# Kernel tuning notes

Hardware: AMD Instinct MI355X
Metric: run time of the kernel (lower is better)

Reference implementation:

```python
import jax, jax.numpy as jnp
import numpy as np

B, S, D = 2, 2048, 2048
H = 16
NOPE, ROPE, DV = 128, 64, 128
DQK = NOPE + ROPE  # 192
QLR, KVLR = 1536, 512


def setup_inputs() -> dict:
    key = jax.random.key(0)
    ks = jax.random.split(key, 8)
    hidden_states = jax.random.normal(ks[0], (B, S, D), dtype=jnp.float32) * 0.02
    sequence_mask = jnp.ones((B, S), dtype=bool)
    # rotary frequencies (complex exponential split into cos/sin), theta=10000
    inv_freq = 1.0 / (10000.0 ** (np.arange(0, ROPE, 2, dtype=np.float32) / ROPE))
    angles = np.outer(np.arange(S, dtype=np.float32), inv_freq)  # [S, ROPE//2]
    freqs_cos = jnp.asarray(np.cos(angles), dtype=jnp.float32)
    freqs_sin = jnp.asarray(np.sin(angles), dtype=jnp.float32)
    def lin(k, fan_in, fan_out):
        return jax.random.normal(k, (fan_in, fan_out), dtype=jnp.float32) / np.sqrt(fan_in)
    return {
        'hidden_states': hidden_states,
        'sequence_mask': sequence_mask,
        'freqs_cos': freqs_cos,
        'freqs_sin': freqs_sin,
        'Wq_down': lin(ks[1], D, QLR),
        'Wkv_down': lin(ks[2], D, KVLR + ROPE),
        'Wq_up': lin(ks[3], QLR, H * DQK),
        'Wkv_up': lin(ks[4], KVLR, H * (DV + NOPE)),
        'Wo': lin(ks[5], H * DV, D),
    }


def _rmsnorm(x, eps=1e-5):
    return x * jax.lax.rsqrt(jnp.mean(x * x, axis=-1, keepdims=True) + eps)


def _apply_rope(x, cos, sin):
    # x: [B,S,H,d] with interleaved (real, imag) pairs; cos/sin: [S, d//2]
    b, s, h, d = x.shape
    xr = x.reshape(b, s, h, d // 2, 2)
    x0, x1 = xr[..., 0], xr[..., 1]
    c = cos[None, :s, None, :]
    sn = sin[None, :s, None, :]
    y = jnp.stack([x0 * c - x1 * sn, x0 * sn + x1 * c], axis=-1)
    return y.reshape(b, s, h, d)


def reference(hidden_states, sequence_mask, freqs_cos, freqs_sin,
              Wq_down, Wkv_down, Wq_up, Wkv_up, Wo):
    b, s, _ = hidden_states.shape
    # Q path: down-project -> rmsnorm -> up-project
    q_latent = _rmsnorm(hidden_states @ Wq_down)
    q = (q_latent @ Wq_up).reshape(b, s, H, DQK)
    q_nope, q_rope = q[..., :NOPE], q[..., NOPE:]
    q_rope = _apply_rope(q_rope, freqs_cos, freqs_sin)
    q = jnp.concatenate([q_rope, q_nope], axis=-1)  # [B,S,H,DQK]
    # KV path
    kvdr = hidden_states @ Wkv_down  # [B,S,KVLR+ROPE]
    kv_latent, k_rope = kvdr[..., :KVLR], kvdr[..., KVLR:]
    k_rope = _apply_rope(k_rope.reshape(b, s, 1, ROPE), freqs_cos, freqs_sin)
    k_rope = jnp.broadcast_to(k_rope, (b, s, H, ROPE))
    kv = _rmsnorm(kv_latent) @ Wkv_up  # [B,S,H*(NOPE+DV)]
    k_nope = kv[..., :H * NOPE].reshape(b, s, H, NOPE)
    v = kv[..., H * NOPE:].reshape(b, s, H, DV)
    k = jnp.concatenate([k_rope, k_nope], axis=-1)  # [B,S,H,DQK]
    # causal attention (flash_attn_varlen with full masks == per-batch causal)
    scale = 1.0 / np.sqrt(DQK)
    scores = jnp.einsum('bqhd,bkhd->bhqk', q, k) * scale
    causal = jnp.tril(jnp.ones((s, s), dtype=bool))
    mask = causal[None, None, :, :] & sequence_mask[:, None, None, :]
    scores = jnp.where(mask, scores, jnp.float32(-1e9))
    attn = jax.nn.softmax(scores, axis=-1)
    out = jnp.einsum('bhqk,bkhd->bqhd', attn, v).reshape(b, s, H * DV)
    return out @ Wo
```

## Files before the change

kernel.cpp:

```cpp
#include <hip/hip_runtime.h>
#include <math.h>


typedef unsigned short u16;
typedef __attribute__((ext_vector_type(8))) __bf16 bf16x8;
typedef __attribute__((ext_vector_type(4))) float f32x4;

#define DEV static __device__ __forceinline__

DEV float b2f(u16 v) { return __uint_as_float(((unsigned int)v) << 16); }
DEV u16 f2b(float f) {
  unsigned int u = __float_as_uint(f);
  u += 0x7fffu + ((u >> 16) & 1u);
  return (u16)(u >> 16);
}

DEV float waveReduceSum(float v) {
  #pragma unroll
  for (int o = 32; o > 0; o >>= 1) v += __shfl_down(v, o, 64);
  return v;
}

DEV void gld16(const u16* g, u16* l) {
  __builtin_amdgcn_global_load_lds((const __attribute__((address_space(1))) void*)g,
                                   (__attribute__((address_space(3))) void*)l, 16, 0, 0);
}

__global__ __launch_bounds__(256)
void cvt_f32_bf16(const float* __restrict__ in, u16* __restrict__ out, int n4) {
  int i = blockIdx.x * 256 + threadIdx.x;
  if (i < n4) {
    float4 v = reinterpret_cast<const float4*>(in)[i];
    ushort4 o;
    o.x = f2b(v.x); o.y = f2b(v.y); o.z = f2b(v.z); o.w = f2b(v.w);
    reinterpret_cast<ushort4*>(out)[i] = o;
  }
}

__global__ __launch_bounds__(256)
void transpose_f32_bf16(const float* __restrict__ in, u16* __restrict__ out, int R, int C) {
  __shared__ u16 tile[32][33];
  int c0 = blockIdx.x * 32, r0 = blockIdx.y * 32;
  for (int i = threadIdx.y; i < 32; i += 8)
    tile[i][threadIdx.x] = f2b(in[(size_t)(r0 + i) * C + c0 + threadIdx.x]);
  __syncthreads();
  for (int i = threadIdx.y; i < 32; i += 8)
    out[(size_t)(c0 + i) * R + r0 + threadIdx.x] = tile[threadIdx.x][i];
}

template<int OUT_BF16>
__global__ __launch_bounds__(256)
void gemm_bt(const u16* __restrict__ A, const u16* __restrict__ BT, void* __restrict__ Cp,
             int M, int N, int K) {
  __shared__ __attribute__((aligned(16))) u16 As[4096];
  __shared__ __attribute__((aligned(16))) u16 Bs[4096];
  const int tid = threadIdx.x;
  const int lane = tid & 63;
  const int wave = tid >> 6;
  const int wm = (wave >> 1) * 64;
  const int wn = (wave & 1) * 64;
  const int q = lane >> 4;
  const int l16 = lane & 15;

  const int gx = gridDim.x;
  const int nwg = gx * gridDim.y;
  const int orig = blockIdx.y * gx + blockIdx.x;
  const int cpx = nwg >> 3;
  const int swz = (orig & 7) * cpx + (orig >> 3);
  const int bm = (swz / gx) * 128;
  const int bn = (swz % gx) * 128;

  f32x4 zero = {0.f, 0.f, 0.f, 0.f};
  f32x4 acc[4][4];
  #pragma unroll
  for (int i = 0; i < 4; i++)
    #pragma unroll
    for (int j = 0; j < 4; j++) acc[i][j] = zero;

  for (int k0 = 0; k0 < K; k0 += 32) {
    #pragma unroll
    for (int i = 0; i < 2; i++) {
      int jb = i * 256 + wave * 64;
      int u = jb + lane;
      int row = u >> 2;
      int kq = (u & 3) ^ ((u >> 3) & 3);
      gld16(A + (size_t)(bm + row) * K + k0 + kq * 8, As + jb * 8);
      int rB = bn + row;
      if (rB >= N) rB = N - 1;
      gld16(BT + (size_t)rB * K + k0 + kq * 8, Bs + jb * 8);
    }
    __syncthreads();
    bf16x8 af[4], bfr[4];
    #pragma unroll
    for (int t = 0; t < 4; t++) {
      int rowA = wm + t * 16 + l16;
      int rowB = wn + t * 16 + l16;
      int uA = (rowA << 2) | (q ^ ((rowA >> 1) & 3));
      int uB = (rowB << 2) | (q ^ ((rowB >> 1) & 3));
      af[t]  = *reinterpret_cast<const bf16x8*>(As + uA * 8);
      bfr[t] = *reinterpret_cast<const bf16x8*>(Bs + uB * 8);
    }
    #pragma unroll
    for (int mt = 0; mt < 4; mt++)
      #pragma unroll
      for (int nt = 0; nt < 4; nt++)
        acc[mt][nt] = __builtin_amdgcn_mfma_f32_16x16x32_bf16(af[mt], bfr[nt], acc[mt][nt], 0, 0, 0);
    __syncthreads();
  }

  float* Cf = (float*)Cp;
  u16* Cb = (u16*)Cp;
  #pragma unroll
  for (int mt = 0; mt < 4; mt++) {
    #pragma unroll
    for (int nt = 0; nt < 4; nt++) {
      int col = bn + wn + nt * 16 + l16;
      if (col < N) {
        int row0 = bm + wm + mt * 16 + q * 4;
        #pragma unroll
        for (int r = 0; r < 4; r++) {
          size_t idx = (size_t)(row0 + r) * N + col;
          float v = acc[mt][nt][r];
          if (OUT_BF16) Cb[idx] = f2b(v); else Cf[idx] = v;
        }
      }
    }
  }
}

__global__ __launch_bounds__(256)
void rmsnorm_rows(const float* __restrict__ in, u16* __restrict__ out, int C, int stride) {
  int row = blockIdx.x;
  const float* x = in + (size_t)row * stride;
  float ss = 0.f;
  for (int i = threadIdx.x; i < C; i += 256) { float v = x[i]; ss += v * v; }
  ss = waveReduceSum(ss);
  __shared__ float red[4];
  __shared__ float s_scale;
  int lane = threadIdx.x & 63, wid = threadIdx.x >> 6;
  if (lane == 0) red[wid] = ss;
  __syncthreads();
  if (threadIdx.x == 0)
    s_scale = rsqrtf((red[0] + red[1] + red[2] + red[3]) / (float)C + 1e-5f);
  __syncthreads();
  float sc = s_scale;
  u16* o = out + (size_t)row * C;
  for (int i = threadIdx.x; i < C; i += 256) o[i] = f2b(x[i] * sc);
}

__global__ __launch_bounds__(256)
void rope_pack_q(const u16* __restrict__ q2, const float* __restrict__ fc, const float* __restrict__ fs,
                 u16* __restrict__ Q) {
  const float scale = 0.07216878364870323f;
  int bs = blockIdx.x;
  int b = bs >> 11, s = bs & 2047;
  __shared__ float c[32], sn[32];
  if (threadIdx.x < 32) {
    c[threadIdx.x] = fc[s * 32 + threadIdx.x];
    sn[threadIdx.x] = fs[s * 32 + threadIdx.x];
  }
  __syncthreads();
  const u16* qrow = q2 + (size_t)bs * 3072;
  for (int t = threadIdx.x; t < 512; t += 256) {
    int h = t >> 5, i = t & 31;
    float x0 = b2f(qrow[h * 192 + 128 + 2 * i]);
    float x1 = b2f(qrow[h * 192 + 128 + 2 * i + 1]);
    size_t base = ((size_t)(b * 16 + h) * 2048 + s) * 192;
    Q[base + 2 * i]     = f2b((x0 * c[i] - x1 * sn[i]) * scale);
    Q[base + 2 * i + 1] = f2b((x0 * sn[i] + x1 * c[i]) * scale);
  }
  for (int t = threadIdx.x; t < 2048; t += 256) {
    int h = t >> 7, j = t & 127;
    Q[((size_t)(b * 16 + h) * 2048 + s) * 192 + 64 + j] = f2b(b2f(qrow[h * 192 + j]) * scale);
  }
}

__global__ __launch_bounds__(256)
void kv_split(const float* __restrict__ t13, const float* __restrict__ fc, const float* __restrict__ fs,
              u16* __restrict__ kvl, u16* __restrict__ krope) {
  int row = blockIdx.x;
  int s = row & 2047;
  const float* x = t13 + (size_t)row * 2112 + 1536;
  float ss = 0.f;
  for (int i = threadIdx.x; i < 512; i += 256) { float v = x[i]; ss += v * v; }
  ss = waveReduceSum(ss);
  __shared__ float red[4];
  __shared__ float s_scale;
  int lane = threadIdx.x & 63, wid = threadIdx.x >> 6;
  if (lane == 0) red[wid] = ss;
  __syncthreads();
  if (threadIdx.x == 0)
    s_scale = rsqrtf((red[0] + red[1] + red[2] + red[3]) * (1.0f / 512.0f) + 1e-5f);
  __syncthreads();
  float sc = s_scale;
  for (int i = threadIdx.x; i < 512; i += 256) kvl[(size_t)row * 512 + i] = f2b(x[i] * sc);
  if (threadIdx.x < 32) {
    int i = threadIdx.x;
    float cc = fc[s * 32 + i], sn = fs[s * 32 + i];
    float x0 = x[512 + 2 * i], x1 = x[512 + 2 * i + 1];
    krope[(size_t)row * 64 + 2 * i]     = f2b(x0 * cc - x1 * sn);
    krope[(size_t)row * 64 + 2 * i + 1] = f2b(x0 * sn + x1 * cc);
  }
}

__global__ __launch_bounds__(256)
void assemble_kv2(const u16* __restrict__ kvb, const u16* __restrict__ krope,
                  u16* __restrict__ Kc, u16* __restrict__ Vt) {
  int ks = blockIdx.x;
  int bh = blockIdx.y;
  int b = bh >> 4, h = bh & 15;
  int t = threadIdx.x;
  if (t < 192) {
    int kq = t >> 3, sl = t & 7;
    int s = ks * 8 + sl;
    size_t bs = (size_t)(b * 2048 + s);
    uint4 v;
    if (kq < 8) v = *reinterpret_cast<const uint4*>(krope + bs * 64 + kq * 8);
    else        v = *reinterpret_cast<const uint4*>(kvb + bs * 4096 + h * 128 + (kq - 8) * 8);
    *reinterpret_cast<uint4*>(Kc + (((size_t)bh * 24 + kq) * 2048 + s) * 8) = v;
  }
  if (t < 128) {
    int dv = t;
    u16 tmp[8];
    #pragma unroll
    for (int j = 0; j < 8; j++) {
      int s = ks * 8 + j;
      tmp[j] = kvb[(size_t)(b * 2048 + s) * 4096 + 2048 + h * 128 + dv];
    }
    *reinterpret_cast<uint4*>(Vt + (((size_t)bh * 256 + ks) * 128 + dv) * 8) = *reinterpret_cast<uint4*>(tmp);
  }
}

__global__ __launch_bounds__(256, 2)
void flash_attn7(const u16* __restrict__ Q, const u16* __restrict__ Kc,
                 const u16* __restrict__ Vt, u16* __restrict__ O) {
  __shared__ __attribute__((aligned(16))) u16 Ks[2][24 * 64 * 8];
  __shared__ __attribute__((aligned(16))) u16 Vs[8 * 128 * 8];
  __shared__ __attribute__((aligned(16))) u16 Ps[4 * 16 * 72];

  const int blk = blockIdx.x;
  const int bh = ((blk & 7) << 2) | (blk >> 7);
  const int tpair = (blk >> 3) & 15;
  const int b = bh >> 4, h = bh & 15;
  const int tid = threadIdx.x, lane = tid & 63, wave = tid >> 6;
  const int quad = lane >> 4, l16 = lane & 15;
  u16* PsW = Ps + wave * 16 * 72;

  bf16x8 onesf;
  #pragma unroll
  for (int j = 0; j < 8; j++) onesf[j] = (l16 == 0) ? (__bf16)1.0f : (__bf16)0.0f;

  auto stageK = [&](u16* KsB, int kk) {
    #pragma unroll
    for (int ii = 0; ii < 6; ii++) {
      int kq = wave * 6 + ii;
      gld16(Kc + (((size_t)bh * 24 + kq) * 2048 + kk + lane) * 8, KsB + kq * 64 * 8);
    }
  };
  auto stageV = [&](int kk) {
    #pragma unroll
    for (int jj = 0; jj < 4; jj++) {
      int vc = wave * 4 + jj, kc = vc >> 1, dvh = vc & 1;
      gld16(Vt + (((size_t)bh * 256 + (kk >> 3) + kc) * 128 + dvh * 64 + lane) * 8,
            Vs + (kc * 128 + dvh * 64) * 8);
    }
  };

  for (int phase = 0; phase < 2; phase++) {
    const int qt = phase == 0 ? tpair : 31 - tpair;
    const int q0 = qt * 64;
    const int nk = (qt + 1) * 64;

    bf16x8 qf[6];
    {
      int qrow = q0 + wave * 16 + l16;
      const u16* qp = Q + ((size_t)bh * 2048 + qrow) * 192 + quad * 8;
      #pragma unroll
      for (int kc = 0; kc < 6; kc++)
        qf[kc] = *reinterpret_cast<const bf16x8*>(qp + kc * 32);
    }

    f32x4 zero = {0.f, 0.f, 0.f, 0.f};
    f32x4 oacc[9];
    #pragma unroll
    for (int nt = 0; nt < 9; nt++) oacc[nt] = zero;

    for (int k0 = 0; k0 < nk; k0 += 64) {
      const int cur = (k0 >> 6) & 1;
      const bool hasnext = (k0 + 64 < nk);

      __builtin_amdgcn_s_barrier();
      __builtin_amdgcn_sched_barrier(0);
      if (k0 == 0) stageK(Ks[0], 0);
      stageV(k0);
      if (hasnext) {
        stageK(Ks[cur ^ 1], k0 + 64);
        asm volatile("s_waitcnt vmcnt(10)" ::: "memory");
      } else {
        asm volatile("s_waitcnt vmcnt(4)" ::: "memory");
      }
      __builtin_amdgcn_sched_barrier(0);
      __builtin_amdgcn_s_barrier();
      __builtin_amdgcn_sched_barrier(0);

      const u16* KsC = Ks[cur];

      f32x4 sacc[4];
      #pragma unroll
      for (int nt = 0; nt < 4; nt++) sacc[nt] = zero;
      #pragma unroll
      for (int kc = 0; kc < 6; kc++) {
        #pragma unroll
        for (int nt = 0; nt < 4; nt++) {
          bf16x8 kb = *reinterpret_cast<const bf16x8*>(KsC + ((kc * 4 + quad) * 64 + nt * 16 + l16) * 8);
          sacc[nt] = __builtin_amdgcn_mfma_f32_16x16x32_bf16(qf[kc], kb, sacc[nt], 0, 0, 0);
        }
      }

      #pragma unroll
      for (int r = 0; r < 4; r++) {
        int qrow_g = q0 + wave * 16 + quad * 4 + r;
        #pragma unroll
        for (int nt = 0; nt < 4; nt++) {
          int key = k0 + nt * 16 + l16;
          float p = (key <= qrow_g) ? __expf(sacc[nt][r]) : 0.f;
          PsW[(quad * 4 + r) * 72 + nt * 16 + l16] = f2b(p);
        }
      }

      if (hasnext) asm volatile("s_waitcnt vmcnt(6)" ::: "memory");
      else         asm volatile("s_waitcnt vmcnt(0)" ::: "memory");
      __builtin_amdgcn_sched_barrier(0);
      __builtin_amdgcn_s_barrier();
      __builtin_amdgcn_sched_barrier(0);

      #pragma unroll
      for (int kcp = 0; kcp < 2; kcp++) {
        bf16x8 pa = *reinterpret_cast<const bf16x8*>(PsW + l16 * 72 + kcp * 32 + quad * 8);
        #pragma unroll
        for (int nt = 0; nt < 8; nt++) {
          bf16x8 vb = *reinterpret_cast<const bf16x8*>(Vs + ((kcp * 4 + quad) * 128 + nt * 16 + l16) * 8);
          oacc[nt] = __builtin_amdgcn_mfma_f32_16x16x32_bf16(pa, vb, oacc[nt], 0, 0, 0);
        }
        oacc[8] = __builtin_amdgcn_mfma_f32_16x16x32_bf16(pa, onesf, oacc[8], 0, 0, 0);
      }
    }

    #pragma unroll
    for (int r = 0; r < 4; r++) {
      float l = __shfl(oacc[8][r], lane & 48, 64);
      float inv = 1.0f / l;
      int s = q0 + wave * 16 + quad * 4 + r;
      #pragma unroll
      for (int nt = 0; nt < 8; nt++)
        O[((size_t)b * 2048 + s) * 2048 + h * 128 + nt * 16 + l16] = f2b(oacc[nt][r] * inv);
    }
  }
}

extern "C" void kernel_launch(void* const* d_in, const int* in_sizes, int n_in,
                              void* d_out, int out_size, void* d_ws, size_t ws_size,
                              hipStream_t stream) {
  (void)in_sizes; (void)n_in; (void)out_size; (void)ws_size;
  const float* hs   = (const float*)d_in[0];
  const float* fc   = (const float*)d_in[2];
  const float* fs   = (const float*)d_in[3];
  const float* Wqd  = (const float*)d_in[4];
  const float* Wkvd = (const float*)d_in[5];
  const float* Wqu  = (const float*)d_in[6];
  const float* Wkvu = (const float*)d_in[7];
  const float* Wo   = (const float*)d_in[8];

  char* ws = (char*)d_ws;
  size_t off = 0;
  auto alloc = [&](size_t bytes) { size_t o = off; off += (bytes + 255) & ~(size_t)255; return o; };
  const size_t oHS   = alloc(16777216);
  const size_t oRA   = alloc(16777216);
  const size_t oRB   = alloc(25165824);
  const size_t oRC   = alloc(12582912);
  const size_t oRD   = alloc(25165824);
  const size_t oRE   = alloc(34603008);
  const size_t oKVL  = alloc(4194304);
  const size_t oKR   = alloc(524288);
  const size_t oW13T  = alloc(8650752);
  const size_t oWquT  = alloc(9437184);
  const size_t oWkvuT = alloc(4194304);
  const size_t oWoT   = alloc(8388608);

  u16* hs_bf = (u16*)(ws + oHS);
  u16* Vt   = (u16*)(ws + oRA);
  u16* q2   = (u16*)(ws + oRB);
  u16* Kc   = (u16*)(ws + oRB);
  u16* qlat = (u16*)(ws + oRC);
  u16* Qb   = (u16*)(ws + oRD);
  float* t13 = (float*)(ws + oRE);
  u16* kvb  = (u16*)(ws + oRE);
  u16* attn_out = (u16*)(ws + oRE);
  u16* kvl  = (u16*)(ws + oKVL);
  u16* krope = (u16*)(ws + oKR);
  u16* W13T  = (u16*)(ws + oW13T);
  u16* WquT  = (u16*)(ws + oWquT);
  u16* WkvuT = (u16*)(ws + oWkvuT);
  u16* WoT   = (u16*)(ws + oWoT);

  cvt_f32_bf16<<<8192, 256, 0, stream>>>(hs, hs_bf, 2097152);
  dim3 tb(32, 8);
  transpose_f32_bf16<<<dim3(48, 64), tb, 0, stream>>>(Wqd, W13T, 2048, 1536);
  transpose_f32_bf16<<<dim3(18, 64), tb, 0, stream>>>(Wkvd, W13T + (size_t)1536 * 2048, 2048, 576);
  transpose_f32_bf16<<<dim3(96, 48), tb, 0, stream>>>(Wqu, WquT, 1536, 3072);
  transpose_f32_bf16<<<dim3(128, 16), tb, 0, stream>>>(Wkvu, WkvuT, 512, 4096);
  transpose_f32_bf16<<<dim3(64, 64), tb, 0, stream>>>(Wo, WoT, 2048, 2048);

  gemm_bt<0><<<dim3(17, 32), 256, 0, stream>>>(hs_bf, W13T, t13, 4096, 2112, 2048);
  rmsnorm_rows<<<4096, 256, 0, stream>>>(t13, qlat, 1536, 2112);
  gemm_bt<1><<<dim3(24, 32), 256, 0, stream>>>(qlat, WquT, q2, 4096, 3072, 1536);
  rope_pack_q<<<4096, 256, 0, stream>>>(q2, fc, fs, Qb);
  kv_split<<<4096, 256, 0, stream>>>(t13, fc, fs, kvl, krope);
  gemm_bt<1><<<dim3(32, 32), 256, 0, stream>>>(kvl, WkvuT, kvb, 4096, 4096, 512);
  assemble_kv2<<<dim3(256, 32), 256, 0, stream>>>(kvb, krope, Kc, Vt);
  flash_attn7<<<dim3(512), 256, 0, stream>>>(Qb, Kc, Vt, attn_out);
  gemm_bt<0><<<dim3(16, 32), 256, 0, stream>>>(attn_out, WoT, (float*)d_out, 4096, 2048, 2048);
}
```

Before: 470.7 us.

## Merge launches, fuse norm kernels, and use exp2 with a mask fast path in attention

Result: faster. 446.2 us (-5.2%).

```diff
diff --git a/kernel.cpp b/kernel.cpp
--- a/kernel.cpp
+++ b/kernel.cpp
@@ -7,12 +7,24 @@
 typedef __attribute__((ext_vector_type(4))) float f32x4;
 
 #define DEV static __device__ __forceinline__
+
+#if __has_builtin(__builtin_amdgcn_exp2f)
+#define EXP2(x) __builtin_amdgcn_exp2f(x)
+#else
+#define EXP2(x) exp2f(x)
+#endif
 
 DEV float b2f(u16 v) { return __uint_as_float(((unsigned int)v) << 16); }
 DEV u16 f2b(float f) {
   unsigned int u = __float_as_uint(f);
   u += 0x7fffu + ((u >> 16) & 1u);
   return (u16)(u >> 16);
+}
+DEV u16 f2b_hw(float f) {
+  __bf16 h = (__bf16)f;
+  u16 r;
+  __builtin_memcpy(&r, &h, 2);
+  return r;
 }
 
 DEV float waveReduceSum(float v) {
@@ -38,9 +50,20 @@
 }
 
 __global__ __launch_bounds__(256)
-void transpose_f32_bf16(const float* __restrict__ in, u16* __restrict__ out, int R, int C) {
+void transpose_all(const float* __restrict__ Wqd, const float* __restrict__ Wkvd,
+                   const float* __restrict__ Wqu, const float* __restrict__ Wkvu,
+                   const float* __restrict__ Wo,
+                   u16* __restrict__ W13T, u16* __restrict__ WquT,
+                   u16* __restrict__ WkvuT, u16* __restrict__ WoT) {
   __shared__ u16 tile[32][33];
-  int c0 = blockIdx.x * 32, r0 = blockIdx.y * 32;
+  int n = blockIdx.x;
+  const float* in; u16* out; int R, C, gx, local;
+  if (n < 3072)       { in = Wqd;  out = W13T;                        R = 2048; C = 1536; gx = 48;  local = n; }
+  else if (n < 4224)  { in = Wkvd; out = W13T + (size_t)1536 * 2048;  R = 2048; C = 576;  gx = 18;  local = n - 3072; }
+  else if (n < 8832)  { in = Wqu;  out = WquT;                        R = 1536; C = 3072; gx = 96;  local = n - 4224; }
+  else if (n < 10880) { in = Wkvu; out = WkvuT;                       R = 512;  C = 4096; gx = 128; local = n - 8832; }
+  else                { in = Wo;   out = WoT;                         R = 2048; C = 2048; gx = 64;  local = n - 10880; }
+  int c0 = (local % gx) * 32, r0 = (local / gx) * 32;
   for (int i = threadIdx.y; i < 32; i += 8)
     tile[i][threadIdx.x] = f2b(in[(size_t)(r0 + i) * C + c0 + threadIdx.x]);
   __syncthreads();
@@ -49,11 +72,8 @@
 }
 
 template<int OUT_BF16>
-__global__ __launch_bounds__(256)
-void gemm_bt(const u16* __restrict__ A, const u16* __restrict__ BT, void* __restrict__ Cp,
-             int M, int N, int K) {
-  __shared__ __attribute__((aligned(16))) u16 As[4096];
-  __shared__ __attribute__((aligned(16))) u16 Bs[4096];
+DEV void gemm_body(const u16* __restrict__ A, const u16* __restrict__ BT, void* __restrict__ Cp,
+                   int N, int K, int gx, int nwg, int orig, u16* As, u16* Bs) {
   const int tid = threadIdx.x;
   const int lane = tid & 63;
   const int wave = tid >> 6;
@@ -62,9 +82,6 @@
   const int q = lane >> 4;
   const int l16 = lane & 15;
 
-  const int gx = gridDim.x;
-  const int nwg = gx * gridDim.y;
-  const int orig = blockIdx.y * gx + blockIdx.x;
   const int cpx = nwg >> 3;
   const int swz = (orig & 7) * cpx + (orig >> 3);
   const int bm = (swz / gx) * 128;
@@ -128,30 +145,76 @@
   }
 }
 
-__global__ __launch_bounds__(256)
-void rmsnorm_rows(const float* __restrict__ in, u16* __restrict__ out, int C, int stride) {
-  int row = blockIdx.x;
-  const float* x = in + (size_t)row * stride;
-  float ss = 0.f;
-  for (int i = threadIdx.x; i < C; i += 256) { float v = x[i]; ss += v * v; }
-  ss = waveReduceSum(ss);
+template<int OUT_BF16>
+__global__ __launch_bounds__(256)
+void gemm_bt(const u16* __restrict__ A, const u16* __restrict__ BT, void* __restrict__ Cp,
+             int N, int K) {
+  __shared__ __attribute__((aligned(16))) u16 As[4096];
+  __shared__ __attribute__((aligned(16))) u16 Bs[4096];
+  const int gx = gridDim.x;
+  const int nwg = gx * gridDim.y;
+  const int orig = blockIdx.y * gx + blockIdx.x;
+  gemm_body<OUT_BF16>(A, BT, Cp, N, K, gx, nwg, orig, As, Bs);
+}
+
+__global__ __launch_bounds__(256)
+void gemm_up2(const u16* __restrict__ qlat, const u16* __restrict__ WquT, u16* __restrict__ q2,
+              const u16* __restrict__ kvl, const u16* __restrict__ WkvuT, u16* __restrict__ kvb) {
+  __shared__ __attribute__((aligned(16))) u16 As[4096];
+  __shared__ __attribute__((aligned(16))) u16 Bs[4096];
+  int n = blockIdx.x;
+  if (n < 768) gemm_body<1>(qlat, WquT, q2, 3072, 1536, 24, 768, n, As, Bs);
+  else         gemm_body<1>(kvl, WkvuT, kvb, 4096, 512, 32, 1024, n - 768, As, Bs);
+}
+
+__global__ __launch_bounds__(256)
+void norm_split(const float* __restrict__ t13, const float* __restrict__ fc, const float* __restrict__ fs,
+                u16* __restrict__ qlat, u16* __restrict__ kvl, u16* __restrict__ krope) {
   __shared__ float red[4];
   __shared__ float s_scale;
   int lane = threadIdx.x & 63, wid = threadIdx.x >> 6;
-  if (lane == 0) red[wid] = ss;
-  __syncthreads();
-  if (threadIdx.x == 0)
-    s_scale = rsqrtf((red[0] + red[1] + red[2] + red[3]) / (float)C + 1e-5f);
-  __syncthreads();
-  float sc = s_scale;
-  u16* o = out + (size_t)row * C;
-  for (int i = threadIdx.x; i < C; i += 256) o[i] = f2b(x[i] * sc);
+  if (blockIdx.x < 4096) {
+    int row = blockIdx.x;
+    const float* x = t13 + (size_t)row * 2112;
+    float ss = 0.f;
+    for (int i = threadIdx.x; i < 1536; i += 256) { float v = x[i]; ss += v * v; }
+    ss = waveReduceSum(ss);
+    if (lane == 0) red[wid] = ss;
+    __syncthreads();
+    if (threadIdx.x == 0)
+      s_scale = rsqrtf((red[0] + red[1] + red[2] + red[3]) * (1.0f / 1536.0f) + 1e-5f);
+    __syncthreads();
+    float sc = s_scale;
+    u16* o = qlat + (size_t)row * 1536;
+    for (int i = threadIdx.x; i < 1536; i += 256) o[i] = f2b(x[i] * sc);
+  } else {
+    int row = blockIdx.x - 4096;
+    int s = row & 2047;
+    const float* x = t13 + (size_t)row * 2112 + 1536;
+    float ss = 0.f;
+    for (int i = threadIdx.x; i < 512; i += 256) { float v = x[i]; ss += v * v; }
+    ss = waveReduceSum(ss);
+    if (lane == 0) red[wid] = ss;
+    __syncthreads();
+    if (threadIdx.x == 0)
+      s_scale = rsqrtf((red[0] + red[1] + red[2] + red[3]) * (1.0f / 512.0f) + 1e-5f);
+    __syncthreads();
+    float sc = s_scale;
+    for (int i = threadIdx.x; i < 512; i += 256) kvl[(size_t)row * 512 + i] = f2b(x[i] * sc);
+    if (threadIdx.x < 32) {
+      int i = threadIdx.x;
+      float cc = fc[s * 32 + i], sn = fs[s * 32 + i];
+      float x0 = x[512 + 2 * i], x1 = x[512 + 2 * i + 1];
+      krope[(size_t)row * 64 + 2 * i]     = f2b(x0 * cc - x1 * sn);
+      krope[(size_t)row * 64 + 2 * i + 1] = f2b(x0 * sn + x1 * cc);
+    }
+  }
 }
 
 __global__ __launch_bounds__(256)
 void rope_pack_q(const u16* __restrict__ q2, const float* __restrict__ fc, const float* __restrict__ fs,
                  u16* __restrict__ Q) {
-  const float scale = 0.07216878364870323f;
+  const float scale = 0.10411756711f;
   int bs = blockIdx.x;
   int b = bs >> 11, s = bs & 2047;
   __shared__ float c[32], sn[32];
@@ -172,34 +235,6 @@
   for (int t = threadIdx.x; t < 2048; t += 256) {
     int h = t >> 7, j = t & 127;
     Q[((size_t)(b * 16 + h) * 2048 + s) * 192 + 64 + j] = f2b(b2f(qrow[h * 192 + j]) * scale);
-  }
-}
-
-__global__ __launch_bounds__(256)
-void kv_split(const float* __restrict__ t13, const float* __restrict__ fc, const float* __restrict__ fs,
-              u16* __restrict__ kvl, u16* __restrict__ krope) {
-  int row = blockIdx.x;
-  int s = row & 2047;
-  const float* x = t13 + (size_t)row * 2112 + 1536;
-  float ss = 0.f;
-  for (int i = threadIdx.x; i < 512; i += 256) { float v = x[i]; ss += v * v; }
-  ss = waveReduceSum(ss);
-  __shared__ float red[4];
-  __shared__ float s_scale;
-  int lane = threadIdx.x & 63, wid = threadIdx.x >> 6;
-  if (lane == 0) red[wid] = ss;
-  __syncthreads();
-  if (threadIdx.x == 0)
-    s_scale = rsqrtf((red[0] + red[1] + red[2] + red[3]) * (1.0f / 512.0f) + 1e-5f);
-  __syncthreads();
-  float sc = s_scale;
-  for (int i = threadIdx.x; i < 512; i += 256) kvl[(size_t)row * 512 + i] = f2b(x[i] * sc);
-  if (threadIdx.x < 32) {
-    int i = threadIdx.x;
-    float cc = fc[s * 32 + i], sn = fs[s * 32 + i];
-    float x0 = x[512 + 2 * i], x1 = x[512 + 2 * i + 1];
-    krope[(size_t)row * 64 + 2 * i]     = f2b(x0 * cc - x1 * sn);
-    krope[(size_t)row * 64 + 2 * i + 1] = f2b(x0 * sn + x1 * cc);
   }
 }
 
@@ -232,7 +267,7 @@
 }
 
 __global__ __launch_bounds__(256, 2)
-void flash_attn7(const u16* __restrict__ Q, const u16* __restrict__ Kc,
+void flash_attn8(const u16* __restrict__ Q, const u16* __restrict__ Kc,
                  const u16* __restrict__ Vt, u16* __restrict__ O) {
   __shared__ __attribute__((aligned(16))) u16 Ks[2][24 * 64 * 8];
   __shared__ __attribute__((aligned(16))) u16 Vs[8 * 128 * 8];
@@ -317,14 +352,26 @@
         }
       }
 
-      #pragma unroll
-      for (int r = 0; r < 4; r++) {
-        int qrow_g = q0 + wave * 16 + quad * 4 + r;
+      if (k0 + 63 <= q0 + wave * 16) {
         #pragma unroll
-        for (int nt = 0; nt < 4; nt++) {
-          int key = k0 + nt * 16 + l16;
-          float p = (key <= qrow_g) ? __expf(sacc[nt][r]) : 0.f;
-          PsW[(quad * 4 + r) * 72 + nt * 16 + l16] = f2b(p);
+        for (int r = 0; r < 4; r++) {
+          #pragma unroll
+          for (int nt = 0; nt < 4; nt++) {
+            float p = EXP2(sacc[nt][r]);
+            PsW[(quad * 4 + r) * 72 + nt * 16 + l16] = f2b_hw(p);
+          }
+        }
+      } else {
+        #pragma unroll
+        for (int r = 0; r < 4; r++) {
+          int qrow_g = q0 + wave * 16 + quad * 4 + r;
+          #pragma unroll
+          for (int nt = 0; nt < 4; nt++) {
+            int key = k0 + nt * 16 + l16;
+            float e = EXP2(sacc[nt][r]);
+            float p = (key <= qrow_g) ? e : 0.f;
+            PsW[(quad * 4 + r) * 72 + nt * 16 + l16] = f2b_hw(p);
+          }
         }
       }
 
@@ -404,20 +451,13 @@
   u16* WoT   = (u16*)(ws + oWoT);
 
   cvt_f32_bf16<<<8192, 256, 0, stream>>>(hs, hs_bf, 2097152);
-  dim3 tb(32, 8);
-  transpose_f32_bf16<<<dim3(48, 64), tb, 0, stream>>>(Wqd, W13T, 2048, 1536);
-  transpose_f32_bf16<<<dim3(18, 64), tb, 0, stream>>>(Wkvd, W13T + (size_t)1536 * 2048, 2048, 576);
-  transpose_f32_bf16<<<dim3(96, 48), tb, 0, stream>>>(Wqu, WquT, 1536, 3072);
-  transpose_f32_bf16<<<dim3(128, 16), tb, 0, stream>>>(Wkvu, WkvuT, 512, 4096);
-  transpose_f32_bf16<<<dim3(64, 64), tb, 0, stream>>>(Wo, WoT, 2048, 2048);
-
-  gemm_bt<0><<<dim3(17, 32), 256, 0, stream>>>(hs_bf, W13T, t13, 4096, 2112, 2048);
-  rmsnorm_rows<<<4096, 256, 0, stream>>>(t13, qlat, 1536, 2112);
-  gemm_bt<1><<<dim3(24, 32), 256, 0, stream>>>(qlat, WquT, q2, 4096, 3072, 1536);
+  transpose_all<<<14976, dim3(32, 8), 0, stream>>>(Wqd, Wkvd, Wqu, Wkvu, Wo, W13T, WquT, WkvuT, WoT);
+
+  gemm_bt<0><<<dim3(17, 32), 256, 0, stream>>>(hs_bf, W13T, t13, 2112, 2048);
+  norm_split<<<8192, 256, 0, stream>>>(t13, fc, fs, qlat, kvl, krope);
+  gemm_up2<<<1792, 256, 0, stream>>>(qlat, WquT, q2, kvl, WkvuT, kvb);
   rope_pack_q<<<4096, 256, 0, stream>>>(q2, fc, fs, Qb);
-  kv_split<<<4096, 256, 0, stream>>>(t13, fc, fs, kvl, krope);
-  gemm_bt<1><<<dim3(32, 32), 256, 0, stream>>>(kvl, WkvuT, kvb, 4096, 4096, 512);
   assemble_kv2<<<dim3(256, 32), 256, 0, stream>>>(kvb, krope, Kc, Vt);
-  flash_attn7<<<dim3(512), 256, 0, stream>>>(Qb, Kc, Vt, attn_out);
-  gemm_bt<0><<<dim3(16, 32), 256, 0, stream>>>(attn_out, WoT, (float*)d_out, 4096, 2048, 2048);
-}
+  flash_attn8<<<dim3(512), 256, 0, stream>>>(Qb, Kc, Vt, attn_out);
+  gemm_bt<0><<<dim3(16, 32), 256, 0, stream>>>(attn_out, WoT, (float*)d_out, 2048, 2048);
+}
```
